# Kernel optimization log

Hardware: AMD Instinct MI355X
Metric: run time of the kernel (lower is better)

The kernel has to match this reference:

```python
import jax, jax.numpy as jnp
import numpy as np

N_HEADS = 16

def setup_inputs() -> dict:
    key = jax.random.key(0)
    ks = jax.random.split(key, 6)
    B, S, D = 2, 2048, 1024
    sc = 0.02
    return {
        "x": jax.random.normal(ks[0], (B, S, D), dtype=jnp.float32),
        "Wq": jax.random.normal(ks[1], (D, D), dtype=jnp.float32) * sc,
        "Wk": jax.random.normal(ks[2], (D, D), dtype=jnp.float32) * sc,
        "Wv": jax.random.normal(ks[3], (D, D), dtype=jnp.float32) * sc,
        "Wo": jax.random.normal(ks[4], (D, D), dtype=jnp.float32) * sc,
        "bo": jnp.zeros((D,), dtype=jnp.float32),
        "stride": 64,
    }

def _strided_mask(S: int, stride: int):
    # local window |i-j|<=1  OR  |i-j| == k*stride (k>=1); diff==0 is in the window
    i = jnp.arange(S)[:, None]
    j = jnp.arange(S)[None, :]
    diff = jnp.abs(i - j)
    return (diff <= 1) | (diff % stride == 0)  # [S, S] bool

def reference(x, Wq, Wk, Wv, Wo, bo, stride):
    B, S, D = x.shape
    H = N_HEADS
    Dh = D // H
    # q/k/v projections: nn.Linear(bias=False) applies x @ W.T
    def proj(W):
        return (x @ W.T).reshape(B, S, H, Dh).transpose(0, 2, 1, 3)  # [B,H,S,Dh]
    q, k, v = proj(Wq), proj(Wk), proj(Wv)
    scores = jnp.einsum('bhqd,bhkd->bhqk', q, k) / jnp.sqrt(jnp.float32(Dh))
    mask = _strided_mask(S, stride)  # [S,S]
    scores = jnp.where(mask[None, None], scores, -jnp.inf)
    attn = jax.nn.softmax(scores, axis=-1)  # dropout is identity in eval
    out = jnp.einsum('bhqk,bhkd->bhqd', attn, v)  # [B,H,S,Dh]
    out = out.transpose(0, 2, 1, 3).reshape(B, S, D)
    return out @ Wo.T + bo
```

## Files before the change

### kernel.cpp

```cpp
#include <hip/hip_runtime.h>
#include <hip/hip_bf16.h>


typedef __bf16 bf16;
typedef __attribute__((ext_vector_type(4))) __bf16 bf16x4;
typedef __attribute__((ext_vector_type(8))) __bf16 bf16x8;
typedef __attribute__((ext_vector_type(4))) float f32x4;
typedef __attribute__((ext_vector_type(4))) unsigned int u32x4;

constexpr int S_ = 2048;
constexpr int D_ = 1024;
constexpr int H_ = 16;
constexpr int DH = 64;
constexpr int M_ = 2 * S_;

__device__ __forceinline__ void gload_lds16(const bf16* g, bf16* l) {
    __builtin_amdgcn_global_load_lds(
        (const __attribute__((address_space(1))) void*)g,
        (__attribute__((address_space(3))) void*)l, 16, 0, 0);
}

#define BARRIER_FULL() do { asm volatile("" ::: "memory"); \
    __builtin_amdgcn_sched_barrier(0); \
    __builtin_amdgcn_s_barrier(); \
    __builtin_amdgcn_sched_barrier(0); \
    asm volatile("" ::: "memory"); } while (0)

#define WAIT_LGKM0() do { asm volatile("s_waitcnt lgkmcnt(0)" ::: "memory"); \
    __builtin_amdgcn_sched_barrier(0); } while (0)

#define WAIT_VM0() do { asm volatile("s_waitcnt vmcnt(0)" ::: "memory"); \
    __builtin_amdgcn_sched_barrier(0); } while (0)

#define WAIT_VM4() do { asm volatile("s_waitcnt vmcnt(4)" ::: "memory"); \
    __builtin_amdgcn_sched_barrier(0); } while (0)

__device__ __forceinline__ void stage64(const bf16* __restrict__ G, int base_row,
                                        int kcol, bf16* lds, int wave, int lane)
{
    const int rIn = lane >> 3;
    const int g   = (lane & 7) ^ rIn;
    #pragma unroll
    for (int l = 0; l < 2; ++l) {
        const int c = wave * 2 + l;
        gload_lds16(G + (size_t)(base_row + c * 8 + rIn) * D_ + kcol + g * 8,
                    lds + c * 512);
    }
}

__global__ __launch_bounds__(512, 1)
void gemm_qkv_8p(const bf16* __restrict__ A,
                 const bf16* __restrict__ W,
                 bf16* __restrict__ C)
{
    constexpr int BK = 64;
    constexpr int NT = D_ / BK;
    constexpr int HS = 128 * BK;
    __shared__ __align__(16) bf16 As[2][2][HS];
    __shared__ __align__(16) bf16 Bs[2][2][HS];

    const int tid  = threadIdx.x;
    const int wave = tid >> 6;
    const int lane = tid & 63;
    const int wm = wave >> 2;
    const int wn = wave & 3;

    const int lid = blockIdx.y * 12 + blockIdx.x;
    const int xcd = lid & 7, pos = lid >> 3;
    const int bxs = (xcd & 1) * 6 + pos % 6;
    const int bys = (xcd >> 1) * 4 + pos / 6;
    const int bm = bys * 256;
    const int bn = bxs * 256;

    const int l15 = lane & 15;
    const int hi  = lane >> 4;
    const int r7  = l15 & 7;
    const int bh  = wn >> 1;

    int aOff[2][4][2], bOff[2][2][2];
    #pragma unroll
    for (int mh = 0; mh < 2; ++mh)
        #pragma unroll
        for (int fm = 0; fm < 4; ++fm)
            #pragma unroll
            for (int kk = 0; kk < 2; ++kk)
                aOff[mh][fm][kk] = (mh * 64 + fm * 16 + l15) * 64
                                 + (((kk * 4 + hi) ^ r7) * 8);
    #pragma unroll
    for (int nh = 0; nh < 2; ++nh)
        #pragma unroll
        for (int fn = 0; fn < 2; ++fn)
            #pragma unroll
            for (int kk = 0; kk < 2; ++kk)
                bOff[nh][fn][kk] = ((wn & 1) * 64 + nh * 32 + fn * 16 + l15) * 64
                                 + (((kk * 4 + hi) ^ r7) * 8);

    f32x4 acc[8][4];
    #pragma unroll
    for (int i = 0; i < 8; ++i)
        #pragma unroll
        for (int j = 0; j < 4; ++j) acc[i][j] = f32x4{0.f, 0.f, 0.f, 0.f};

    bf16x8 aF[4][2], bF0[2][2], bF1[2][2];

#define Q16(MH, NH, BF) do { _Pragma("unroll") \
    for (int fm = 0; fm < 4; ++fm) { _Pragma("unroll") \
        for (int fn = 0; fn < 2; ++fn) { _Pragma("unroll") \
            for (int kk = 0; kk < 2; ++kk) \
                acc[(MH)*4+fm][(NH)*2+fn] = __builtin_amdgcn_mfma_f32_16x16x32_bf16( \
                    aF[fm][kk], BF[fn][kk], acc[(MH)*4+fm][(NH)*2+fn], 0, 0, 0); \
    } } } while (0)

    stage64(A, bm +   0, 0,  &As[0][0][0], wave, lane);
    stage64(A, bm + 128, 0,  &As[0][1][0], wave, lane);
    stage64(W, bn +   0, 0,  &Bs[0][0][0], wave, lane);
    stage64(W, bn + 128, 0,  &Bs[0][1][0], wave, lane);
    stage64(W, bn +   0, BK, &Bs[1][0][0], wave, lane);
    stage64(A, bm +   0, BK, &As[1][0][0], wave, lane);
    WAIT_VM4();
    BARRIER_FULL();

    for (int t = 0; t < NT; ++t) {
        const int d = t & 1;
        const bf16* aH = &As[d][wm][0];
        const bf16* bH = &Bs[d][bh][0];
        const bool pre1 = (t + 1) < NT;
        const bool pre2 = (t + 2) < NT;
        const int k1 = (t + 1) * BK, k2 = (t + 2) * BK;

        #pragma unroll
        for (int fn = 0; fn < 2; ++fn)
            #pragma unroll
            for (int kk = 0; kk < 2; ++kk)
                bF0[fn][kk] = *(const bf16x8*)(bH + bOff[0][fn][kk]);
        #pragma unroll
        for (int fm = 0; fm < 4; ++fm)
            #pragma unroll
            for (int kk = 0; kk < 2; ++kk)
                aF[fm][kk] = *(const bf16x8*)(aH + aOff[0][fm][kk]);
        if (pre1) stage64(A, bm + 128, k1, &As[d ^ 1][1][0], wave, lane);
        BARRIER_FULL(); WAIT_LGKM0();
        __builtin_amdgcn_s_setprio(1); Q16(0, 0, bF0); __builtin_amdgcn_s_setprio(0);
        BARRIER_FULL();

        #pragma unroll
        for (int fn = 0; fn < 2; ++fn)
            #pragma unroll
            for (int kk = 0; kk < 2; ++kk)
                bF1[fn][kk] = *(const bf16x8*)(bH + bOff[1][fn][kk]);
        if (pre1) stage64(W, bn + 128, k1, &Bs[d ^ 1][1][0], wave, lane);
        BARRIER_FULL(); WAIT_LGKM0();
        __builtin_amdgcn_s_setprio(1); Q16(0, 1, bF1); __builtin_amdgcn_s_setprio(0);
        BARRIER_FULL();

        #pragma unroll
        for (int fm = 0; fm < 4; ++fm)
            #pragma unroll
            for (int kk = 0; kk < 2; ++kk)
                aF[fm][kk] = *(const bf16x8*)(aH + aOff[1][fm][kk]);
        if (pre2) stage64(W, bn + 0, k2, &Bs[d][0][0], wave, lane);
        BARRIER_FULL(); WAIT_LGKM0();
        __builtin_amdgcn_s_setprio(1); Q16(1, 1, bF1); __builtin_amdgcn_s_setprio(0);
        BARRIER_FULL();

        if (pre2) stage64(A, bm + 0, k2, &As[d][0][0], wave, lane);
        __builtin_amdgcn_s_setprio(1); Q16(1, 0, bF0); __builtin_amdgcn_s_setprio(0);
        if (pre2) { WAIT_VM4(); } else { WAIT_VM0(); }
        BARRIER_FULL();
    }
#undef Q16

    #pragma unroll
    for (int i = 0; i < 8; ++i) {
        #pragma unroll
        for (int j = 0; j < 4; ++j) {
            const int n = bn + wn * 64 + j * 16 + l15;
            bf16* Cz = C + (size_t)(n >> 10) * M_ * D_;
            const int col = n & 1023;
            const int mb = bm + wm * 128 + i * 16 + hi * 4;
            #pragma unroll
            for (int r2 = 0; r2 < 4; ++r2)
                Cz[(size_t)(mb + r2) * D_ + col] = (bf16)acc[i][j][r2];
        }
    }
}

__global__ __launch_bounds__(512, 1)
void gemm_o_2ph(const bf16* __restrict__ A,
                const bf16* __restrict__ W,
                float* __restrict__ Cf,
                const float* __restrict__ bias)
{
    constexpr int BK = 64;
    constexpr int NT = D_ / BK;
    constexpr int TSLOT = 128 * BK;
    __shared__ __align__(16) bf16 As[3 * TSLOT];
    __shared__ __align__(16) bf16 Bs[3 * TSLOT];

    const int tid  = threadIdx.x;
    const int wave = tid >> 6;
    const int lane = tid & 63;
    const int wm = wave >> 2;
    const int wn = wave & 3;

    const int lid = blockIdx.y * 8 + blockIdx.x;
    const int xcd = lid & 7, pos = lid >> 3;
    const int bxs = (xcd & 3) * 2 + (pos & 1);
    const int bys = (xcd >> 2) * 16 + (pos >> 1);
    const int bm = bys * 128;
    const int bn = bxs * 128;

    const int l15 = lane & 15;
    const int hi  = lane >> 4;
    const int r7  = l15 & 7;

    int aOff[2][4], bOff[2][2];
    #pragma unroll
    for (int ks = 0; ks < 2; ++ks) {
        #pragma unroll
        for (int fm = 0; fm < 4; ++fm)
            aOff[ks][fm] = (wm * 64 + fm * 16 + l15) * 64 + (((ks * 4 + hi) ^ r7) * 8);
        #pragma unroll
        for (int fn = 0; fn < 2; ++fn)
            bOff[ks][fn] = (wn * 32 + fn * 16 + l15) * 64 + (((ks * 4 + hi) ^ r7) * 8);
    }

    f32x4 acc[4][2];
    #pragma unroll
    for (int i = 0; i < 4; ++i)
        #pragma unroll
        for (int j = 0; j < 2; ++j) acc[i][j] = f32x4{0.f, 0.f, 0.f, 0.f};

    bf16x8 aF0[4], aF1[4], bF[2][2];

    stage64(A, bm, 0,  As,         wave, lane);
    stage64(W, bn, 0,  Bs,         wave, lane);
    stage64(A, bm, BK, As + TSLOT, wave, lane);
    stage64(W, bn, BK, Bs + TSLOT, wave, lane);
    WAIT_VM4();
    BARRIER_FULL();

    int cur = 0;
    for (int t = 0; t < NT; ++t) {
        const int ss = (cur + 2 >= 3) ? (cur - 1) : (cur + 2);
        const bf16* aslot = As + cur * TSLOT;
        const bf16* bslot = Bs + cur * TSLOT;
        const bool pre = (t + 2) < NT;
        const int kn = (t + 2) * BK;

        #pragma unroll
        for (int ks = 0; ks < 2; ++ks)
            #pragma unroll
            for (int fn = 0; fn < 2; ++fn)
                bF[ks][fn] = *(const bf16x8*)(bslot + bOff[ks][fn]);
        #pragma unroll
        for (int fm = 0; fm < 4; ++fm)
            aF0[fm] = *(const bf16x8*)(aslot + aOff[0][fm]);
        if (pre) stage64(A, bm, kn, As + ss * TSLOT, wave, lane);
        BARRIER_FULL(); WAIT_LGKM0();
        __builtin_amdgcn_s_setprio(1);
        #pragma unroll
        for (int fm = 0; fm < 4; ++fm)
            #pragma unroll
            for (int fn = 0; fn < 2; ++fn)
                acc[fm][fn] = __builtin_amdgcn_mfma_f32_16x16x32_bf16(
                    aF0[fm], bF[0][fn], acc[fm][fn], 0, 0, 0);
        __builtin_amdgcn_s_setprio(0);
        BARRIER_FULL();

        #pragma unroll
        for (int fm = 0; fm < 4; ++fm)
            aF1[fm] = *(const bf16x8*)(aslot + aOff[1][fm]);
        if (pre) stage64(W, bn, kn, Bs + ss * TSLOT, wave, lane);
        BARRIER_FULL(); WAIT_LGKM0();
        __builtin_amdgcn_s_setprio(1);
        #pragma unroll
        for (int fm = 0; fm < 4; ++fm)
            #pragma unroll
            for (int fn = 0; fn < 2; ++fn)
                acc[fm][fn] = __builtin_amdgcn_mfma_f32_16x16x32_bf16(
                    aF1[fm], bF[1][fn], acc[fm][fn], 0, 0, 0);
        __builtin_amdgcn_s_setprio(0);
        if (pre) { WAIT_VM4(); } else { WAIT_VM0(); }
        BARRIER_FULL();
        cur = (cur + 1 >= 3) ? 0 : (cur + 1);
    }

    #pragma unroll
    for (int fm = 0; fm < 4; ++fm) {
        #pragma unroll
        for (int fn = 0; fn < 2; ++fn) {
            const int n = bn + wn * 32 + fn * 16 + l15;
            const float bv = bias[n];
            const int mb = bm + wm * 64 + fm * 16 + hi * 4;
            #pragma unroll
            for (int r2 = 0; r2 < 4; ++r2)
                Cf[(size_t)(mb + r2) * D_ + n] = acc[fm][fn][r2] + bv;
        }
    }
}

template<bool AF32, bool BF32, bool CF32, bool BIAS>
__global__ __launch_bounds__(256)
void gemm_bt(const void* __restrict__ Av,
             const void* __restrict__ W0v, const void* __restrict__ W1v,
             const void* __restrict__ W2v,
             void* __restrict__ Cv, const float* __restrict__ bias)
{
    constexpr int BM = 128, BK = 64;
    constexpr int N = D_, K = D_;
    __shared__ __align__(16) bf16 As[BM * BK];
    __shared__ __align__(16) bf16 Bs[BM * BK];

    const int z = blockIdx.z;
    const void* Wv_ = (z == 0) ? W0v : (z == 1) ? W1v : W2v;

    const int tid  = threadIdx.x;
    const int wave = tid >> 6;
    const int lane = tid & 63;

    const int bm = blockIdx.y * BM;
    const int bn = blockIdx.x * BM;
    const int wr = wave >> 1;
    const int wc = wave & 1;

    f32x4 acc[4][4];
    #pragma unroll
    for (int i = 0; i < 4; ++i)
        #pragma unroll
        for (int j = 0; j < 4; ++j)
            acc[i][j] = f32x4{0.f, 0.f, 0.f, 0.f};

    const int ldRow = lane >> 3;
    const int ldCol = (lane & 7) * 8;

    for (int kt = 0; kt < K; kt += BK) {
        if (AF32) {
            const float* A = (const float*)Av;
            #pragma unroll
            for (int it = 0; it < 8; ++it) {
                const int flat = (it * 256 + tid) * 4;
                const int row = flat >> 6, col = flat & 63;
                const float4 v = *(const float4*)(A + (size_t)(bm + row) * K + kt + col);
                bf16x4 p = { (bf16)v.x, (bf16)v.y, (bf16)v.z, (bf16)v.w };
                *(bf16x4*)&As[row * BK + col] = p;
            }
        } else {
            const bf16* A = (const bf16*)Av;
            #pragma unroll
            for (int q = 0; q < 4; ++q) {
                const int c = wave * 4 + q;
                const int row = c * 8 + ldRow;
                gload_lds16(A + (size_t)(bm + row) * K + kt + ldCol, &As[c * 8 * BK]);
            }
        }
        if (BF32) {
            const float* W = (const float*)Wv_;
            #pragma unroll
            for (int it = 0; it < 8; ++it) {
                const int flat = (it * 256 + tid) * 4;
                const int row = flat >> 6, col = flat & 63;
                const float4 v = *(const float4*)(W + (size_t)(bn + row) * K + kt + col);
                bf16x4 p = { (bf16)v.x, (bf16)v.y, (bf16)v.z, (bf16)v.w };
                *(bf16x4*)&Bs[row * BK + col] = p;
            }
        } else {
            const bf16* W = (const bf16*)Wv_;
            #pragma unroll
            for (int q = 0; q < 4; ++q) {
                const int c = wave * 4 + q;
                const int row = c * 8 + ldRow;
                gload_lds16(W + (size_t)(bn + row) * K + kt + ldCol, &Bs[c * 8 * BK]);
            }
        }
        __syncthreads();
        #pragma unroll
        for (int kk = 0; kk < 2; ++kk) {
            const int k0 = kk * 32 + (lane >> 4) * 8;
            bf16x8 af[4], bfv[4];
            #pragma unroll
            for (int mi = 0; mi < 4; ++mi)
                af[mi] = *(const bf16x8*)&As[(wr * 64 + mi * 16 + (lane & 15)) * BK + k0];
            #pragma unroll
            for (int ni = 0; ni < 4; ++ni)
                bfv[ni] = *(const bf16x8*)&Bs[(wc * 64 + ni * 16 + (lane & 15)) * BK + k0];
            #pragma unroll
            for (int mi = 0; mi < 4; ++mi)
                #pragma unroll
                for (int ni = 0; ni < 4; ++ni)
                    acc[mi][ni] = __builtin_amdgcn_mfma_f32_16x16x32_bf16(
                        af[mi], bfv[ni], acc[mi][ni], 0, 0, 0);
        }
        __syncthreads();
    }

    #pragma unroll
    for (int mi = 0; mi < 4; ++mi) {
        #pragma unroll
        for (int ni = 0; ni < 4; ++ni) {
            const int n  = bn + wc * 64 + ni * 16 + (lane & 15);
            const int mb = bm + wr * 64 + mi * 16 + (lane >> 4) * 4;
            float bv = 0.f;
            if (BIAS) bv = bias[n];
            #pragma unroll
            for (int r2 = 0; r2 < 4; ++r2) {
                const int m = mb + r2;
                if (CF32) {
                    ((float*)Cv)[(size_t)m * N + n] = acc[mi][ni][r2] + bv;
                } else {
                    bf16* Cc = (bf16*)Cv + (size_t)z * M_ * D_;
                    Cc[(size_t)m * N + n] = (bf16)(acc[mi][ni][r2] + bv);
                }
            }
        }
    }
}

__global__ __launch_bounds__(256)
void convert_to_bf16(const float* __restrict__ x,
                     const float* __restrict__ w0, const float* __restrict__ w1,
                     const float* __restrict__ w2, const float* __restrict__ w3,
                     bf16* __restrict__ out)
{
    const size_t eid = ((size_t)blockIdx.x * 256 + threadIdx.x) * 8;
    const float* src; size_t off;
    if (eid < (size_t)(1u << 22)) { src = x; off = eid; }
    else {
        const size_t t = eid - (1u << 22);
        const int k = (int)(t >> 20);
        off = t & ((1u << 20) - 1);
        src = (k == 0) ? w0 : (k == 1) ? w1 : (k == 2) ? w2 : w3;
    }
    const float4 a = *(const float4*)(src + off);
    const float4 c = *(const float4*)(src + off + 4);
    bf16x8 v = { (bf16)a.x, (bf16)a.y, (bf16)a.z, (bf16)a.w,
                 (bf16)c.x, (bf16)c.y, (bf16)c.z, (bf16)c.w };
    *(bf16x8*)(out + eid) = v;
}

__device__ __forceinline__ unsigned pk2bf(float lo, float hi) {
    const unsigned a = __builtin_bit_cast(unsigned short, (bf16)lo);
    const unsigned b = __builtin_bit_cast(unsigned short, (bf16)hi);
    return a | (b << 16);
}

__global__ __launch_bounds__(256)
void attn_mfma(bf16* __restrict__ QA, const bf16* __restrict__ Kw,
               const bf16* __restrict__ Vw)
{
    constexpr int WSLOT = 4096 + 8320;
    __shared__ __align__(16) unsigned char smem[4 * WSLOT];

    const int lane = threadIdx.x & 63;
    const int wv   = threadIdx.x >> 6;
    const int wid  = blockIdx.x * 4 + wv;
    const int r = wid & 63;
    const int h = (wid >> 6) & (H_ - 1);
    const int b = wid >> 10;

    const int qlo = lane & 15;
    const int g   = lane >> 4;
    const size_t rb = (size_t)b * S_;
    const int col0 = h * DH;
    const float scale = 0.125f;

    unsigned char* ws = smem + wv * WSLOT;
    bf16*  vlds = (bf16*)ws;
    float* bnce = (float*)(ws + 4096);

    {
        const int krow = lane >> 3;
        const int slot = lane & 7;
        #pragma unroll
        for (int i = 0; i < 4; ++i) {
            const int k = i * 8 + krow;
            gload_lds16(Vw + (rb + (size_t)(r + 64 * k)) * D_ + col0
                           + ((slot ^ (k & 7)) * 8),
                        vlds + i * 512);
        }
    }

    f32x4 accS[2][2];
    #pragma unroll
    for (int a = 0; a < 2; ++a)
        #pragma unroll
        for (int c = 0; c < 2; ++c) accS[a][c] = f32x4{0.f,0.f,0.f,0.f};

    #pragma unroll
    for (int c = 0; c < 2; ++c) {
        bf16x8 kf[2], qf[2];
        #pragma unroll
        for (int t = 0; t < 2; ++t) {
            const size_t row = rb + (size_t)(r + 64 * (t * 16 + qlo));
            kf[t] = *(const bf16x8*)&Kw[row * D_ + col0 + c * 32 + g * 8];
            qf[t] = *(const bf16x8*)&QA[row * D_ + col0 + c * 32 + g * 8];
        }
        #pragma unroll
        for (int kt = 0; kt < 2; ++kt)
            #pragma unroll
            for (int qt = 0; qt < 2; ++qt)
                accS[kt][qt] = __builtin_amdgcn_mfma_f32_16x16x32_bf16(
                    kf[kt], qf[qt], accS[kt][qt], 0, 0, 0);
    }

    const int s_nb = lane & 31;
    const int side = lane >> 5;
    const int i_nb = r + 64 * s_nb;
    const int j_nb = side ? (i_nb + 1) : (i_nb - 1);
    const bool nbv = (unsigned)j_nb < (unsigned)S_;
    const int j_sf = nbv ? j_nb : i_nb;
    float nbd = 0.f;
    #pragma unroll
    for (int t = 0; t < 8; ++t) {
        const bf16x8 qv = *(const bf16x8*)&QA[(rb + i_nb) * D_ + col0 + t * 8];
        const bf16x8 kv = *(const bf16x8*)&Kw[(rb + j_sf) * D_ + col0 + t * 8];
        #pragma unroll
        for (int e = 0; e < 8; ++e) nbd += (float)qv[e] * (float)kv[e];
    }
    const float NEGINF = -__builtin_inff();
    float nb = nbv ? nbd * scale : NEGINF;

    float mx[2] = { NEGINF, NEGINF };
    #pragma unroll
    for (int kt = 0; kt < 2; ++kt)
        #pragma unroll
        for (int qt = 0; qt < 2; ++qt)
            #pragma unroll
            for (int rr = 0; rr < 4; ++rr)
                mx[qt] = fmaxf(mx[qt], accS[kt][qt][rr]);
    mx[0] *= scale; mx[1] *= scale;
    mx[g & 1] = fmaxf(mx[g & 1], nb);
    #pragma unroll
    for (int x = 16; x <= 32; x <<= 1) {
        mx[0] = fmaxf(mx[0], __shfl_xor(mx[0], x));
        mx[1] = fmaxf(mx[1], __shfl_xor(mx[1], x));
    }
    float p[2][2][4];
    float sm[2] = { 0.f, 0.f };
    #pragma unroll
    for (int kt = 0; kt < 2; ++kt)
        #pragma unroll
        for (int qt = 0; qt < 2; ++qt)
            #pragma unroll
            for (int rr = 0; rr < 4; ++rr) {
                const float e = __expf(accS[kt][qt][rr] * scale - mx[qt]);
                p[kt][qt][rr] = e;
                sm[qt] += e;
            }
    float nbp = __expf(nb - mx[g & 1]);
    sm[g & 1] += nbp;
    #pragma unroll
    for (int x = 16; x <= 32; x <<= 1) {
        sm[0] += __shfl_xor(sm[0], x);
        sm[1] += __shfl_xor(sm[1], x);
    }
    const float inv[2] = { 1.f / sm[0], 1.f / sm[1] };
    #pragma unroll
    for (int kt = 0; kt < 2; ++kt)
        #pragma unroll
        for (int qt = 0; qt < 2; ++qt)
            #pragma unroll
            for (int rr = 0; rr < 4; ++rr) p[kt][qt][rr] *= inv[qt];
    nbp *= inv[g & 1];

    unsigned pk_[2][2][2];
    #pragma unroll
    for (int qt = 0; qt < 2; ++qt)
        #pragma unroll
        for (int kt = 0; kt < 2; ++kt)
            #pragma unroll
            for (int w = 0; w < 2; ++w)
                pk_[qt][kt][w] = pk2bf(p[kt][qt][2 * w], p[kt][qt][2 * w + 1]);

    const int srcA = qlo + 32 * (g & 1);
    const int srcB = srcA + 16;
    const int kts  = g >> 1;
    bf16x8 pa[2];
    #pragma unroll
    for (int qt = 0; qt < 2; ++qt) {
        u32x4 fr;
        #pragma unroll
        for (int w = 0; w < 2; ++w) {
            const unsigned a0 = (unsigned)__shfl((int)pk_[qt][0][w], srcA);
            const unsigned a1 = (unsigned)__shfl((int)pk_[qt][1][w], srcA);
            fr[w] = kts ? a1 : a0;
            const unsigned b0 = (unsigned)__shfl((int)pk_[qt][0][w], srcB);
            const unsigned b1 = (unsigned)__shfl((int)pk_[qt][1][w], srcB);
            fr[2 + w] = kts ? b1 : b0;
        }
        pa[qt] = __builtin_bit_cast(bf16x8, fr);
    }

    WAIT_VM0();
    f32x4 accO[2][4];
    #pragma unroll
    for (int qt = 0; qt < 2; ++qt)
        #pragma unroll
        for (int dt = 0; dt < 4; ++dt) accO[qt][dt] = f32x4{0.f,0.f,0.f,0.f};
    #pragma unroll
    for (int dt = 0; dt < 4; ++dt) {
        bf16x8 vf;
        const int sbase = dt * 2 + (qlo >> 3);
        const int boff  = (qlo & 7) * 2;
        #pragma unroll
        for (int e = 0; e < 8; ++e) {
            const int k = g * 8 + e;
            const unsigned short u = *(const unsigned short*)
                ((const unsigned char*)vlds + k * 128 + ((sbase ^ (k & 7)) * 16) + boff);
            vf[e] = __builtin_bit_cast(bf16, u);
        }
        accO[0][dt] = __builtin_amdgcn_mfma_f32_16x16x32_bf16(pa[0], vf, accO[0][dt], 0, 0, 0);
        accO[1][dt] = __builtin_amdgcn_mfma_f32_16x16x32_bf16(pa[1], vf, accO[1][dt], 0, 0, 0);
    }

    #pragma unroll
    for (int qt = 0; qt < 2; ++qt)
        #pragma unroll
        for (int rr = 0; rr < 4; ++rr) {
            const int q = qt * 16 + g * 4 + rr;
            #pragma unroll
            for (int dt = 0; dt < 4; ++dt)
                bnce[q * 65 + dt * 16 + qlo] = accO[qt][dt][rr];
        }
    WAIT_LGKM0();

    for (int q = 0; q < 32; ++q) {
        const float pm = __shfl(nbp, q);
        const float pp = __shfl(nbp, q + 32);
        const int iq = r + 64 * q;
        const int jm = iq > 0 ? iq - 1 : 0;
        const int jp = iq < S_ - 1 ? iq + 1 : S_ - 1;
        float o = bnce[q * 65 + lane];
        o += pm * (float)Vw[(rb + jm) * D_ + col0 + lane];
        o += pp * (float)Vw[(rb + jp) * D_ + col0 + lane];
        QA[(rb + iq) * D_ + col0 + lane] = (bf16)o;
    }
}

extern "C" void kernel_launch(void* const* d_in, const int* in_sizes, int n_in,
                              void* d_out, int out_size, void* d_ws, size_t ws_size,
                              hipStream_t stream)
{
    const float* x  = (const float*)d_in[0];
    const float* Wq = (const float*)d_in[1];
    const float* Wk = (const float*)d_in[2];
    const float* Wv = (const float*)d_in[3];
    const float* Wo = (const float*)d_in[4];
    const float* bo = (const float*)d_in[5];

    bf16* qws = (bf16*)d_ws;
    bf16* kws = qws + (size_t)M_ * D_;
    bf16* vws = kws + (size_t)M_ * D_;

    const bool fast = ws_size >= (size_t)40 * 1024 * 1024;

    if (fast) {
        bf16* xb  = vws + (size_t)M_ * D_;
        bf16* wqb = xb + (1u << 22);
        bf16* wob = wqb + 3 * (1u << 20);

        convert_to_bf16<<<4096, 256, 0, stream>>>(x, Wq, Wk, Wv, Wo, xb);

        gemm_qkv_8p<<<dim3(3 * D_ / 256, M_ / 256), 512, 0, stream>>>(xb, wqb, qws);

        attn_mfma<<<dim3(2 * H_ * 64 / 4), 256, 0, stream>>>(qws, kws, vws);

        gemm_o_2ph<<<dim3(D_ / 128, M_ / 128), 512, 0, stream>>>(
            qws, wob, (float*)d_out, bo);
    } else {
        gemm_bt<true, true, false, false><<<dim3(D_/128, M_/128, 3), 256, 0, stream>>>(
            x, Wq, Wk, Wv, qws, nullptr);

        attn_mfma<<<dim3(2 * H_ * 64 / 4), 256, 0, stream>>>(qws, kws, vws);

        gemm_bt<false, true, true, true><<<dim3(D_/128, M_/128, 1), 256, 0, stream>>>(
            qws, Wo, nullptr, nullptr, (float*)d_out, bo);
    }
}
```

Measured before the change: 84.62 us.

## Replace 256x256 8-phase QKV GEMM with 128x128 double-buffered tiles

```diff
diff --git a/kernel.cpp b/kernel.cpp
--- a/kernel.cpp
+++ b/kernel.cpp
@@ -48,16 +48,16 @@
     }
 }
 
-__global__ __launch_bounds__(512, 1)
-void gemm_qkv_8p(const bf16* __restrict__ A,
+__global__ __launch_bounds__(512, 4)
+void gemm_qkv_db(const bf16* __restrict__ A,
                  const bf16* __restrict__ W,
                  bf16* __restrict__ C)
 {
     constexpr int BK = 64;
     constexpr int NT = D_ / BK;
-    constexpr int HS = 128 * BK;
-    __shared__ __align__(16) bf16 As[2][2][HS];
-    __shared__ __align__(16) bf16 Bs[2][2][HS];
+    constexpr int TSLOT = 128 * BK;
+    __shared__ __align__(16) bf16 As[2 * TSLOT];
+    __shared__ __align__(16) bf16 Bs[2 * TSLOT];
 
     const int tid  = threadIdx.x;
     const int wave = tid >> 6;
@@ -65,122 +65,98 @@
     const int wm = wave >> 2;
     const int wn = wave & 3;
 
-    const int lid = blockIdx.y * 12 + blockIdx.x;
+    const int lid = blockIdx.y * 24 + blockIdx.x;
     const int xcd = lid & 7, pos = lid >> 3;
-    const int bxs = (xcd & 1) * 6 + pos % 6;
-    const int bys = (xcd >> 1) * 4 + pos / 6;
-    const int bm = bys * 256;
-    const int bn = bxs * 256;
+    const int bxs = (xcd & 1) * 12 + pos % 12;
+    const int bys = (xcd >> 1) * 8 + pos / 12;
+    const int bm = bys * 128;
+    const int bn = bxs * 128;
 
     const int l15 = lane & 15;
     const int hi  = lane >> 4;
     const int r7  = l15 & 7;
-    const int bh  = wn >> 1;
-
-    int aOff[2][4][2], bOff[2][2][2];
-    #pragma unroll
-    for (int mh = 0; mh < 2; ++mh)
-        #pragma unroll
-        for (int fm = 0; fm < 4; ++fm)
-            #pragma unroll
-            for (int kk = 0; kk < 2; ++kk)
-                aOff[mh][fm][kk] = (mh * 64 + fm * 16 + l15) * 64
-                                 + (((kk * 4 + hi) ^ r7) * 8);
-    #pragma unroll
-    for (int nh = 0; nh < 2; ++nh)
+
+    int aOff[2][4], bOff[2][2];
+    #pragma unroll
+    for (int ks = 0; ks < 2; ++ks) {
+        #pragma unroll
+        for (int fm = 0; fm < 4; ++fm)
+            aOff[ks][fm] = (wm * 64 + fm * 16 + l15) * 64 + (((ks * 4 + hi) ^ r7) * 8);
         #pragma unroll
         for (int fn = 0; fn < 2; ++fn)
-            #pragma unroll
-            for (int kk = 0; kk < 2; ++kk)
-                bOff[nh][fn][kk] = ((wn & 1) * 64 + nh * 32 + fn * 16 + l15) * 64
-                                 + (((kk * 4 + hi) ^ r7) * 8);
-
-    f32x4 acc[8][4];
-    #pragma unroll
-    for (int i = 0; i < 8; ++i)
-        #pragma unroll
-        for (int j = 0; j < 4; ++j) acc[i][j] = f32x4{0.f, 0.f, 0.f, 0.f};
-
-    bf16x8 aF[4][2], bF0[2][2], bF1[2][2];
-
-#define Q16(MH, NH, BF) do { _Pragma("unroll") \
-    for (int fm = 0; fm < 4; ++fm) { _Pragma("unroll") \
-        for (int fn = 0; fn < 2; ++fn) { _Pragma("unroll") \
-            for (int kk = 0; kk < 2; ++kk) \
-                acc[(MH)*4+fm][(NH)*2+fn] = __builtin_amdgcn_mfma_f32_16x16x32_bf16( \
-                    aF[fm][kk], BF[fn][kk], acc[(MH)*4+fm][(NH)*2+fn], 0, 0, 0); \
-    } } } while (0)
-
-    stage64(A, bm +   0, 0,  &As[0][0][0], wave, lane);
-    stage64(A, bm + 128, 0,  &As[0][1][0], wave, lane);
-    stage64(W, bn +   0, 0,  &Bs[0][0][0], wave, lane);
-    stage64(W, bn + 128, 0,  &Bs[0][1][0], wave, lane);
-    stage64(W, bn +   0, BK, &Bs[1][0][0], wave, lane);
-    stage64(A, bm +   0, BK, &As[1][0][0], wave, lane);
-    WAIT_VM4();
+            bOff[ks][fn] = (wn * 32 + fn * 16 + l15) * 64 + (((ks * 4 + hi) ^ r7) * 8);
+    }
+
+    f32x4 acc[4][2];
+    #pragma unroll
+    for (int i = 0; i < 4; ++i)
+        #pragma unroll
+        for (int j = 0; j < 2; ++j) acc[i][j] = f32x4{0.f, 0.f, 0.f, 0.f};
+
+    bf16x8 aF0[4], aF1[4], bF[2][2];
+
+    stage64(A, bm, 0, As, wave, lane);
+    stage64(W, bn, 0, Bs, wave, lane);
+    WAIT_VM0();
     BARRIER_FULL();
 
     for (int t = 0; t < NT; ++t) {
         const int d = t & 1;
-        const bf16* aH = &As[d][wm][0];
-        const bf16* bH = &Bs[d][bh][0];
-        const bool pre1 = (t + 1) < NT;
-        const bool pre2 = (t + 2) < NT;
-        const int k1 = (t + 1) * BK, k2 = (t + 2) * BK;
-
-        #pragma unroll
-        for (int fn = 0; fn < 2; ++fn)
-            #pragma unroll
-            for (int kk = 0; kk < 2; ++kk)
-                bF0[fn][kk] = *(const bf16x8*)(bH + bOff[0][fn][kk]);
-        #pragma unroll
-        for (int fm = 0; fm < 4; ++fm)
-            #pragma unroll
-            for (int kk = 0; kk < 2; ++kk)
-                aF[fm][kk] = *(const bf16x8*)(aH + aOff[0][fm][kk]);
-        if (pre1) stage64(A, bm + 128, k1, &As[d ^ 1][1][0], wave, lane);
+        const bf16* aslot = As + d * TSLOT;
+        const bf16* bslot = Bs + d * TSLOT;
+        bf16* ase = As + (d ^ 1) * TSLOT;
+        bf16* bse = Bs + (d ^ 1) * TSLOT;
+        const bool pre = (t + 1) < NT;
+        const int kn = (t + 1) * BK;
+
+        #pragma unroll
+        for (int ks = 0; ks < 2; ++ks)
+            #pragma unroll
+            for (int fn = 0; fn < 2; ++fn)
+                bF[ks][fn] = *(const bf16x8*)(bslot + bOff[ks][fn]);
+        #pragma unroll
+        for (int fm = 0; fm < 4; ++fm)
+            aF0[fm] = *(const bf16x8*)(aslot + aOff[0][fm]);
+        if (pre) stage64(A, bm, kn, ase, wave, lane);
         BARRIER_FULL(); WAIT_LGKM0();
-        __builtin_amdgcn_s_setprio(1); Q16(0, 0, bF0); __builtin_amdgcn_s_setprio(0);
+        __builtin_amdgcn_s_setprio(1);
+        #pragma unroll
+        for (int fm = 0; fm < 4; ++fm)
+            #pragma unroll
+            for (int fn = 0; fn < 2; ++fn)
+                acc[fm][fn] = __builtin_amdgcn_mfma_f32_16x16x32_bf16(
+                    aF0[fm], bF[0][fn], acc[fm][fn], 0, 0, 0);
+        __builtin_amdgcn_s_setprio(0);
         BARRIER_FULL();
 
         #pragma unroll
-        for (int fn = 0; fn < 2; ++fn)
-            #pragma unroll
-            for (int kk = 0; kk < 2; ++kk)
-                bF1[fn][kk] = *(const bf16x8*)(bH + bOff[1][fn][kk]);
-        if (pre1) stage64(W, bn + 128, k1, &Bs[d ^ 1][1][0], wave, lane);
+        for (int fm = 0; fm < 4; ++fm)
+            aF1[fm] = *(const bf16x8*)(aslot + aOff[1][fm]);
+        if (pre) stage64(W, bn, kn, bse, wave, lane);
         BARRIER_FULL(); WAIT_LGKM0();
-        __builtin_amdgcn_s_setprio(1); Q16(0, 1, bF1); __builtin_amdgcn_s_setprio(0);
+        __builtin_amdgcn_s_setprio(1);
+        #pragma unroll
+        for (int fm = 0; fm < 4; ++fm)
+            #pragma unroll
+            for (int fn = 0; fn < 2; ++fn)
+                acc[fm][fn] = __builtin_amdgcn_mfma_f32_16x16x32_bf16(
+                    aF1[fm], bF[1][fn], acc[fm][fn], 0, 0, 0);
+        __builtin_amdgcn_s_setprio(0);
+        WAIT_VM0();
         BARRIER_FULL();
-
-        #pragma unroll
-        for (int fm = 0; fm < 4; ++fm)
-            #pragma unroll
-            for (int kk = 0; kk < 2; ++kk)
-                aF[fm][kk] = *(const bf16x8*)(aH + aOff[1][fm][kk]);
-        if (pre2) stage64(W, bn + 0, k2, &Bs[d][0][0], wave, lane);
-        BARRIER_FULL(); WAIT_LGKM0();
-        __builtin_amdgcn_s_setprio(1); Q16(1, 1, bF1); __builtin_amdgcn_s_setprio(0);
-        BARRIER_FULL();
-
-        if (pre2) stage64(A, bm + 0, k2, &As[d][0][0], wave, lane);
-        __builtin_amdgcn_s_setprio(1); Q16(1, 0, bF0); __builtin_amdgcn_s_setprio(0);
-        if (pre2) { WAIT_VM4(); } else { WAIT_VM0(); }
-        BARRIER_FULL();
-    }
-#undef Q16
-
-    #pragma unroll
-    for (int i = 0; i < 8; ++i) {
-        #pragma unroll
-        for (int j = 0; j < 4; ++j) {
-            const int n = bn + wn * 64 + j * 16 + l15;
+    }
+
+    #pragma unroll
+    for (int fm = 0; fm < 4; ++fm) {
+        #pragma unroll
+        for (int fn = 0; fn < 2; ++fn) {
+            const int n = bn + wn * 32 + fn * 16 + l15;
             bf16* Cz = C + (size_t)(n >> 10) * M_ * D_;
             const int col = n & 1023;
-            const int mb = bm + wm * 128 + i * 16 + hi * 4;
+            const int mb = bm + wm * 64 + fm * 16 + hi * 4;
             #pragma unroll
             for (int r2 = 0; r2 < 4; ++r2)
-                Cz[(size_t)(mb + r2) * D_ + col] = (bf16)acc[i][j][r2];
+                Cz[(size_t)(mb + r2) * D_ + col] = (bf16)acc[fm][fn][r2];
         }
     }
 }
@@ -661,7 +637,7 @@
 
         convert_to_bf16<<<4096, 256, 0, stream>>>(x, Wq, Wk, Wv, Wo, xb);
 
-        gemm_qkv_8p<<<dim3(3 * D_ / 256, M_ / 256), 512, 0, stream>>>(xb, wqb, qws);
+        gemm_qkv_db<<<dim3(3 * D_ / 128, M_ / 128), 512, 0, stream>>>(xb, wqb, qws);
 
         attn_mfma<<<dim3(2 * H_ * 64 / 4), 256, 0, stream>>>(qws, kws, vws);
 
```

New measurement: 83.50 us (median of 2 runs). No clear change (-1.3%).
